# Kernel tuning notes

Measured on AMD Instinct MI355X. Metric: run time of the kernel, lower is better.

## Reference

```python
import jax, jax.numpy as jnp
import numpy as np


def setup_inputs() -> dict:
    key = jax.random.key(0)
    ks = jax.random.split(key, 10)
    N, E, IN, H, OUT = 100000, 1250000, 64, 128, 64
    inp = {
        "x": jax.random.normal(ks[0], (N, IN), dtype=jnp.float32),
        "edge_index": jax.random.randint(ks[1], (2, E), 0, N, dtype=jnp.int64),
        "W1x": jax.random.normal(ks[2], (IN, H), dtype=jnp.float32) * 0.1,
        "b1x": jnp.zeros((H,), jnp.float32),
        "W2x": jax.random.normal(ks[3], (H, H), dtype=jnp.float32) * 0.1,
        "b2x": jnp.zeros((H,), jnp.float32),
        "W1a": jax.random.normal(ks[4], (IN, H), dtype=jnp.float32) * 0.1,
        "b1a": jnp.zeros((H,), jnp.float32),
        "W2a": jax.random.normal(ks[5], (H, H), dtype=jnp.float32) * 0.1,
        "b2a": jnp.zeros((H,), jnp.float32),
        "Wc": jax.random.normal(ks[6], (2 * H, H), dtype=jnp.float32) * 0.1,
        "bc": jnp.zeros((H,), jnp.float32),
        "Wcls": jax.random.normal(ks[7], (H, OUT), dtype=jnp.float32) * 0.1,
        "bcls": jnp.zeros((OUT,), jnp.float32),
        "num_nodes": N,
    }
    return inp


def _normalize_adj(edge_index, num_nodes):
    # add self loops, then D^{-1/2} A D^{-1/2} edge weights (deg counted on rows)
    loops = jnp.arange(num_nodes, dtype=edge_index.dtype)
    ei = jnp.concatenate([edge_index, jnp.stack([loops, loops])], axis=1)
    row, col = ei[0], ei[1]
    deg = jax.ops.segment_sum(jnp.ones(row.shape[0], jnp.float32), row,
                              num_segments=num_nodes)
    dinv = jnp.where(deg > 0, jax.lax.rsqrt(deg), 0.0)
    ew = dinv[row] * dinv[col]
    return row, col, ew


def reference(x, edge_index, W1x, b1x, W2x, b2x, W1a, b1a, W2a, b2a,
              Wc, bc, Wcls, bcls, num_nodes):
    row, col, ew = _normalize_adj(edge_index, num_nodes)
    # sparse adjacency aggregation: gather, scale, scatter-add
    agg = jax.ops.segment_sum(x[col] * ew[:, None], row, num_segments=num_nodes)
    # dual-branch MLPs
    h_x = jax.nn.relu(x @ W1x + b1x) @ W2x + b2x
    h_a = jax.nn.relu(agg @ W1a + b1a) @ W2a + b2a
    h = jnp.concatenate([h_x, h_a], axis=1) @ Wc + bc
    h = jax.nn.relu(h)  # dropout: eval mode (identity)
    return h @ Wcls + bcls
```

## Files before the change

kernel.cpp:

```cpp
#include <hip/hip_runtime.h>
#include <stdint.h>

typedef unsigned short u16;
typedef unsigned int u32;
typedef __attribute__((ext_vector_type(8))) short frag_ab;
typedef __attribute__((ext_vector_type(4))) float f32x4;

__device__ __forceinline__ u16 f2b(float f) {
  unsigned u = __float_as_uint(f);
  return (u16)((u + 0x7fffu + ((u >> 16) & 1u)) >> 16);
}
__device__ __forceinline__ float b2f(u16 u) {
  return __uint_as_float(((unsigned)u) << 16);
}


__global__ void k_detect(const int* __restrict__ ei, int* __restrict__ flag) {
  int t = threadIdx.x;
  int v = ei[2 * t + 1];
  unsigned long long b = __ballot(v == 0);
  if (t == 0) *flag = (b == ~0ULL) ? 1 : 0;
}

__device__ __forceinline__ int edge_at(const void* ei, long pos, int is64) {
  if (is64) return (int)((const long long*)ei)[pos];
  return ((const int*)ei)[pos];
}

__global__ __launch_bounds__(256) void k_bhist_cvt(
    const void* __restrict__ ei, int E, int CH, int NB, int NBpad,
    int* __restrict__ bh, const int* __restrict__ flag,
    const float* __restrict__ x, u16* __restrict__ xb, long n64) {
  __shared__ int cnt[512];
  const int k = blockIdx.x, tid = threadIdx.x;
  for (long i = ((long)k * 256 + tid) * 8; i < n64; i += 65536L * 8) {
    float4 v0 = *(const float4*)(x + i);
    float4 v1 = *(const float4*)(x + i + 4);
    frag_ab o;
    o[0] = (short)f2b(v0.x); o[1] = (short)f2b(v0.y);
    o[2] = (short)f2b(v0.z); o[3] = (short)f2b(v0.w);
    o[4] = (short)f2b(v1.x); o[5] = (short)f2b(v1.y);
    o[6] = (short)f2b(v1.z); o[7] = (short)f2b(v1.w);
    *(frag_ab*)(xb + i) = o;
  }
  int is64 = *flag;
  for (int t = tid; t < NB; t += 256) cnt[t] = 0;
  __syncthreads();
  int e0 = k * CH, e1 = min(E, e0 + CH);
  for (int e = e0 + tid; e < e1; e += 256)
    atomicAdd(&cnt[edge_at(ei, e, is64) >> 9], 1);
  __syncthreads();
  for (int t = tid; t < NB; t += 256) bh[k * NBpad + t] = cnt[t];
}

__global__ __launch_bounds__(256) void k_cscan(
    int* __restrict__ bh, int* __restrict__ bstart, int NB, int NBpad, int E) {
  __shared__ int s[256];
  const int b = threadIdx.x;
  int tot = 0;
  if (b < NB)
    for (int k = 0; k < 256; ++k) tot += bh[k * NBpad + b];
  s[b] = (b < NB) ? tot : 0;
  __syncthreads();
  for (int off = 1; off < 256; off <<= 1) {
    int u = (b >= off) ? s[b - off] : 0;
    __syncthreads();
    s[b] += u;
    __syncthreads();
  }
  int excl = s[b] - tot;
  if (b < NB) {
    bstart[b] = excl;
    int run = excl;
    for (int k = 0; k < 256; ++k) {
      int t = bh[k * NBpad + b];
      bh[k * NBpad + b] = run;
      run += t;
    }
  }
  if (b == 0) bstart[NB] = E;
}

__global__ __launch_bounds__(256) void k_partition(
    const void* __restrict__ ei, int E, int CH, int NB, int NBpad,
    const int* __restrict__ bh, u32* __restrict__ staged,
    const int* __restrict__ flag) {
  __shared__ int cur[512];
  const int k = blockIdx.x, tid = threadIdx.x;
  int is64 = *flag;
  for (int t = tid; t < NB; t += 256) cur[t] = bh[k * NBpad + t];
  __syncthreads();
  int e0 = k * CH, e1 = min(E, e0 + CH);
  for (int e = e0 + tid; e < e1; e += 256) {
    int r = edge_at(ei, e, is64);
    int c = edge_at(ei, (long)E + e, is64);
    int pos = atomicAdd(&cur[r >> 9], 1);
    staged[pos] = ((u32)(r & 511) << 23) | (u32)c;
  }
}

__global__ __launch_bounds__(1024) void k_csr_bucket(
    const u32* __restrict__ staged, const int* __restrict__ bstart,
    int* __restrict__ rowptr, float* __restrict__ dinv,
    u32* __restrict__ cols, int N, int E) {
  __shared__ int cnt[512];
  __shared__ int cur[512];
  const int b = blockIdx.x, tid = threadIdx.x;
  const int r0 = b << 9;
  if (tid < 512) cnt[tid] = 0;
  __syncthreads();
  const int j0 = bstart[b], j1 = bstart[b + 1];
  for (int j = j0 + tid; j < j1; j += 1024)
    atomicAdd(&cnt[staged[j] >> 23], 1);
  __syncthreads();
  if (tid < 512) cur[tid] = cnt[tid];
  __syncthreads();
  for (int off = 1; off < 512; off <<= 1) {
    int v = 0;
    if (tid < 512 && tid >= off) v = cur[tid - off];
    __syncthreads();
    if (tid < 512) cur[tid] += v;
    __syncthreads();
  }
  int myStart = 0;
  if (tid < 512) {
    myStart = j0 + cur[tid] - cnt[tid];
    int r = r0 + tid;
    if (r < N) {
      rowptr[r] = myStart;
      dinv[r] = rsqrtf((float)cnt[tid] + 1.0f);
    }
  }
  __syncthreads();
  if (tid < 512) cur[tid] = myStart;
  if (b == 0 && tid == 0) rowptr[N] = E;
  __syncthreads();
  for (int j = j0 + tid; j < j1; j += 1024) {
    u32 v = staged[j];
    int rl = v >> 23;
    int pos = atomicAdd(&cur[rl], 1);
    cols[pos] = v & 0x7FFFFF;
  }
}

__global__ __launch_bounds__(256) void k_aggregate(
    const int* __restrict__ rowptr, const u32* __restrict__ cols,
    const u16* __restrict__ xb, const float* __restrict__ dinv,
    u16* __restrict__ aggb, int N) {
  int r = (blockIdx.x * 256 + threadIdx.x) >> 6;
  int f = threadIdx.x & 63;
  if (r >= N) return;
  int j = rowptr[r], end = rowptr[r + 1];
  float dr = dinv[r];
  float acc = b2f(xb[(long)r * 64 + f]) * dr;
  for (; j + 4 <= end; j += 4) {
    int c0 = cols[j], c1 = cols[j + 1], c2 = cols[j + 2], c3 = cols[j + 3];
    float w0 = dinv[c0], w1 = dinv[c1], w2 = dinv[c2], w3 = dinv[c3];
    float x0 = b2f(xb[(long)c0 * 64 + f]);
    float x1 = b2f(xb[(long)c1 * 64 + f]);
    float x2 = b2f(xb[(long)c2 * 64 + f]);
    float x3 = b2f(xb[(long)c3 * 64 + f]);
    acc = fmaf(x0, w0, acc);
    acc = fmaf(x1, w1, acc);
    acc = fmaf(x2, w2, acc);
    acc = fmaf(x3, w3, acc);
  }
  for (; j < end; ++j) {
    int c = cols[j];
    acc = fmaf(b2f(xb[(long)c * 64 + f]), dinv[c], acc);
  }
  aggb[(long)r * 64 + f] = f2b(acc * dr);
}

__global__ void k_wprod(const float* __restrict__ W2x, const float* __restrict__ W2a,
                        const float* __restrict__ Wc, const float* __restrict__ b2x,
                        const float* __restrict__ b2a, const float* __restrict__ bc,
                        float* __restrict__ Wxp, float* __restrict__ Wap,
                        float* __restrict__ bp) {
  int b = blockIdx.x, t = threadIdx.x;
  if (b < 128) {
    int j = t & 127;
    bool isX = (t < 128);
    const float* wrow = isX ? (W2x + b * 128) : (W2a + b * 128);
    const float* wc = isX ? Wc : (Wc + 128 * 128);
    float s = 0.f;
    for (int m = 0; m < 128; ++m) s = fmaf(wrow[m], wc[m * 128 + j], s);
    (isX ? Wxp : Wap)[b * 128 + j] = s;
  } else if (t < 128) {
    float s = bc[t];
    for (int m = 0; m < 128; ++m)
      s += b2x[m] * Wc[m * 128 + t] + b2a[m] * Wc[(128 + m) * 128 + t];
    bp[t] = s;
  }
}

__global__ void k_packall(
    const float* __restrict__ W1x, const float* __restrict__ W1a,
    const float* __restrict__ Wxp, const float* __restrict__ Wap,
    const float* __restrict__ Wcls,
    u16* __restrict__ W1xf, u16* __restrict__ W1af,
    u16* __restrict__ Wxpf, u16* __restrict__ Wapf, u16* __restrict__ Wclsf) {
  int blk = blockIdx.x;
  const float* W;
  u16* dst;
  int K, Nc, i0;
  if (blk < 32)       { W = W1x;  dst = W1xf;  K = 64;  Nc = 128; i0 = blk; }
  else if (blk < 64)  { W = W1a;  dst = W1af;  K = 64;  Nc = 128; i0 = blk - 32; }
  else if (blk < 128) { W = Wxp;  dst = Wxpf;  K = 128; Nc = 128; i0 = blk - 64; }
  else if (blk < 192) { W = Wap;  dst = Wapf;  K = 128; Nc = 128; i0 = blk - 128; }
  else                { W = Wcls; dst = Wclsf; K = 128; Nc = 64;  i0 = blk - 192; }
  int i = i0 * 256 + threadIdx.x;
  if (i >= K * Nc) return;
  int b = i & 7, l = (i >> 3) & 63, f = i >> 9;
  int KB = K >> 5;
  int kb = f % KB, nb = f / KB;
  int k = kb * 32 + (l >> 4) * 8 + b;
  int n = nb * 16 + (l & 15);
  dst[i] = f2b(W[k * Nc + n]);
}

__global__ __launch_bounds__(256) void k_mlp(
    const u16* __restrict__ xb, const u16* __restrict__ aggb,
    const u16* __restrict__ W1xf, const u16* __restrict__ W1af,
    const float* __restrict__ b1x, const float* __restrict__ b1a,
    const u16* __restrict__ Wxpf, const u16* __restrict__ Wapf,
    const float* __restrict__ bp,
    const u16* __restrict__ Wclsf, const float* __restrict__ bcls,
    float* __restrict__ out, int N) {
  __shared__ u16 H1[4][16 * 256];
  __shared__ u16 H2[4][16 * 128];
  const int w = threadIdx.x >> 6;
  const int lane = threadIdx.x & 63;
  const int m0 = blockIdx.x * 64 + w * 16;
  const int lm = lane & 15;
  const int lq = lane >> 4;
  u16* h1 = H1[w];
  u16* h2 = H2[w];

  for (int br = 0; br < 2; ++br) {
    const u16* A = br ? aggb : xb;
    const u16* Wf = br ? W1af : W1xf;
    const float* bias = br ? b1a : b1x;
    const u16* ap = A + (long)(m0 + lm) * 64 + lq * 8;
    frag_ab a0 = *(const frag_ab*)(ap);
    frag_ab a1 = *(const frag_ab*)(ap + 32);
#pragma unroll
    for (int nb = 0; nb < 8; ++nb) {
      frag_ab b0 = *(const frag_ab*)(Wf + (size_t)((nb * 2 + 0) * 64 + lane) * 8);
      frag_ab b1v = *(const frag_ab*)(Wf + (size_t)((nb * 2 + 1) * 64 + lane) * 8);
      f32x4 acc = {0.f, 0.f, 0.f, 0.f};
      acc = __builtin_amdgcn_mfma_f32_16x16x32_bf16(a0, b0, acc, 0, 0, 0);
      acc = __builtin_amdgcn_mfma_f32_16x16x32_bf16(a1, b1v, acc, 0, 0, 0);
      int col = nb * 16 + lm;
      float bv = bias[col];
#pragma unroll
      for (int r = 0; r < 4; ++r) {
        int row = lq * 4 + r;
        h1[(row * 256 + br * 128 + col) ^ ((row & 7) << 3)] =
            f2b(fmaxf(acc[r] + bv, 0.f));
      }
    }
  }
  __syncthreads();

  frag_ab hfr[8];
#pragma unroll
  for (int kb = 0; kb < 8; ++kb)
    hfr[kb] = *(const frag_ab*)&h1[(lm * 256 + kb * 32 + lq * 8) ^ ((lm & 7) << 3)];
#pragma unroll
  for (int nb = 0; nb < 8; ++nb) {
    f32x4 acc = {0.f, 0.f, 0.f, 0.f};
#pragma unroll
    for (int kb = 0; kb < 8; ++kb) {
      const u16* Wf2 = (kb < 4) ? Wxpf : Wapf;
      frag_ab b = *(const frag_ab*)(Wf2 + (size_t)((nb * 4 + (kb & 3)) * 64 + lane) * 8);
      acc = __builtin_amdgcn_mfma_f32_16x16x32_bf16(hfr[kb], b, acc, 0, 0, 0);
    }
    int col = nb * 16 + lm;
    float bv = bp[col];
#pragma unroll
    for (int r = 0; r < 4; ++r) {
      int row = lq * 4 + r;
      h2[(row * 128 + col) ^ ((row & 7) << 3)] = f2b(fmaxf(acc[r] + bv, 0.f));
    }
  }
  __syncthreads();

  frag_ab h3[4];
#pragma unroll
  for (int kb = 0; kb < 4; ++kb)
    h3[kb] = *(const frag_ab*)&h2[(lm * 128 + kb * 32 + lq * 8) ^ ((lm & 7) << 3)];
#pragma unroll
  for (int nb = 0; nb < 4; ++nb) {
    f32x4 acc = {0.f, 0.f, 0.f, 0.f};
#pragma unroll
    for (int kb = 0; kb < 4; ++kb) {
      frag_ab b = *(const frag_ab*)(Wclsf + (size_t)((nb * 4 + kb) * 64 + lane) * 8);
      acc = __builtin_amdgcn_mfma_f32_16x16x32_bf16(h3[kb], b, acc, 0, 0, 0);
    }
    int col = nb * 16 + lm;
    float bv = bcls[col];
#pragma unroll
    for (int r = 0; r < 4; ++r) {
      int grow = m0 + lq * 4 + r;
      if (grow < N) out[(long)grow * 64 + col] = acc[r] + bv;
    }
  }
}

extern "C" void kernel_launch(void* const* d_in, const int* in_sizes, int n_in,
                              void* d_out, int out_size, void* d_ws, size_t ws_size,
                              hipStream_t stream) {
  const float* x    = (const float*)d_in[0];
  const void*  ei   = d_in[1];
  const float* W1x  = (const float*)d_in[2];
  const float* b1x  = (const float*)d_in[3];
  const float* W2x  = (const float*)d_in[4];
  const float* b2x  = (const float*)d_in[5];
  const float* W1a  = (const float*)d_in[6];
  const float* b1a  = (const float*)d_in[7];
  const float* W2a  = (const float*)d_in[8];
  const float* b2a  = (const float*)d_in[9];
  const float* Wc   = (const float*)d_in[10];
  const float* bc   = (const float*)d_in[11];
  const float* Wcls = (const float*)d_in[12];
  const float* bcls = (const float*)d_in[13];
  const int N = in_sizes[0] / 64;
  const int E = in_sizes[1] / 2;

  const int NB = (N + 511) >> 9;
  const int NBpad = (NB + 63) & ~63;
  const int CH = (E + 255) / 256;

  float* ws = (float*)d_ws;
  long nAlign = (N + 255) & ~255L;
  float* dinv = ws;
  int*   rowptr = (int*)(ws + nAlign);
  int*   flag = (int*)(ws + 2 * nAlign + 256);
  u16*   xb   = (u16*)(ws + 2 * nAlign + 512);
  u16*   aggb = xb + (long)N * 64;
  float* Wxp  = (float*)(aggb + (long)N * 64);
  float* Wap  = Wxp + 16384;
  float* bp   = Wap + 16384;
  u16*   W1xf = (u16*)(bp + 128);
  u16*   W1af = W1xf + 8192;
  u16*   Wxpf = W1af + 8192;
  u16*   Wapf = Wxpf + 16384;
  u16*   Wclsf = Wapf + 16384;
  int*   bh   = (int*)(Wclsf + 8192);
  int*   bstart = bh + 256 * NBpad;
  u32*   staged = (u32*)(bstart + NB + 64);
  u32*   cols   = staged + E;
  float* out = (float*)d_out;

  k_detect<<<1, 64, 0, stream>>>((const int*)ei, flag);
  k_bhist_cvt<<<256, 256, 0, stream>>>(ei, E, CH, NB, NBpad, bh, flag,
                                       x, xb, (long)N * 64);
  k_cscan<<<1, 256, 0, stream>>>(bh, bstart, NB, NBpad, E);
  k_partition<<<256, 256, 0, stream>>>(ei, E, CH, NB, NBpad, bh, staged, flag);
  k_csr_bucket<<<NB, 1024, 0, stream>>>(staged, bstart, rowptr, dinv, cols, N, E);
  k_aggregate<<<(N * 64 + 255) / 256, 256, 0, stream>>>(rowptr, cols, xb, dinv, aggb, N);
  k_wprod<<<129, 256, 0, stream>>>(W2x, W2a, Wc, b2x, b2a, bc, Wxp, Wap, bp);
  k_packall<<<224, 256, 0, stream>>>(W1x, W1a, Wxp, Wap, Wcls,
                                     W1xf, W1af, Wxpf, Wapf, Wclsf);
  k_mlp<<<(N + 63) / 64, 256, 0, stream>>>(xb, aggb, W1xf, W1af, b1x, b1a,
                                           Wxpf, Wapf, bp, Wclsf, bcls, out, N);
}
```

Measured before the change: 172.8 us.

## Inline int64 detection, fuse weight product with packing, aggregate two rows per wave

Removes the separate detect kernel by having each edge-reading kernel probe the index width itself with a wave ballot. Merges the weight-product and packing kernels into one that writes packed bf16 directly, dropping the fp32 intermediates. The aggregation kernel now gives each wave two rows and interleaves their gathers to raise memory-level parallelism. Together this cuts two launches and should hide more gather latency, at the cost of extra registers and imbalance when the two rows differ in degree.

```diff
diff --git a/kernel.cpp b/kernel.cpp
--- a/kernel.cpp
+++ b/kernel.cpp
@@ -14,12 +14,10 @@
   return __uint_as_float(((unsigned)u) << 16);
 }
 
-
-__global__ void k_detect(const int* __restrict__ ei, int* __restrict__ flag) {
-  int t = threadIdx.x;
-  int v = ei[2 * t + 1];
+__device__ __forceinline__ int detect64(const int* __restrict__ ei32) {
+  int v = ei32[2 * (threadIdx.x & 63) + 1];
   unsigned long long b = __ballot(v == 0);
-  if (t == 0) *flag = (b == ~0ULL) ? 1 : 0;
+  return (b == ~0ULL) ? 1 : 0;
 }
 
 __device__ __forceinline__ int edge_at(const void* ei, long pos, int is64) {
@@ -29,10 +27,11 @@
 
 __global__ __launch_bounds__(256) void k_bhist_cvt(
     const void* __restrict__ ei, int E, int CH, int NB, int NBpad,
-    int* __restrict__ bh, const int* __restrict__ flag,
+    int* __restrict__ bh,
     const float* __restrict__ x, u16* __restrict__ xb, long n64) {
   __shared__ int cnt[512];
   const int k = blockIdx.x, tid = threadIdx.x;
+  const int is64 = detect64((const int*)ei);
   for (long i = ((long)k * 256 + tid) * 8; i < n64; i += 65536L * 8) {
     float4 v0 = *(const float4*)(x + i);
     float4 v1 = *(const float4*)(x + i + 4);
@@ -43,7 +42,6 @@
     o[6] = (short)f2b(v1.z); o[7] = (short)f2b(v1.w);
     *(frag_ab*)(xb + i) = o;
   }
-  int is64 = *flag;
   for (int t = tid; t < NB; t += 256) cnt[t] = 0;
   __syncthreads();
   int e0 = k * CH, e1 = min(E, e0 + CH);
@@ -83,11 +81,10 @@
 
 __global__ __launch_bounds__(256) void k_partition(
     const void* __restrict__ ei, int E, int CH, int NB, int NBpad,
-    const int* __restrict__ bh, u32* __restrict__ staged,
-    const int* __restrict__ flag) {
+    const int* __restrict__ bh, u32* __restrict__ staged) {
   __shared__ int cur[512];
   const int k = blockIdx.x, tid = threadIdx.x;
-  int is64 = *flag;
+  const int is64 = detect64((const int*)ei);
   for (int t = tid; t < NB; t += 256) cur[t] = bh[k * NBpad + t];
   __syncthreads();
   int e0 = k * CH, e1 = min(E, e0 + CH);
@@ -147,76 +144,113 @@
     const int* __restrict__ rowptr, const u32* __restrict__ cols,
     const u16* __restrict__ xb, const float* __restrict__ dinv,
     u16* __restrict__ aggb, int N) {
-  int r = (blockIdx.x * 256 + threadIdx.x) >> 6;
+  int q = (blockIdx.x * 256 + threadIdx.x) >> 6;
   int f = threadIdx.x & 63;
-  if (r >= N) return;
-  int j = rowptr[r], end = rowptr[r + 1];
-  float dr = dinv[r];
-  float acc = b2f(xb[(long)r * 64 + f]) * dr;
-  for (; j + 4 <= end; j += 4) {
-    int c0 = cols[j], c1 = cols[j + 1], c2 = cols[j + 2], c3 = cols[j + 3];
-    float w0 = dinv[c0], w1 = dinv[c1], w2 = dinv[c2], w3 = dinv[c3];
+  int r0 = q * 2, r1 = q * 2 + 1;
+  if (r0 >= N) return;
+  const bool has1 = (r1 < N);
+  int j0 = rowptr[r0], e0 = rowptr[r0 + 1];
+  int j1 = has1 ? rowptr[r1] : 0;
+  int e1 = has1 ? rowptr[r1 + 1] : 0;
+  float d0 = dinv[r0];
+  float d1 = has1 ? dinv[r1] : 0.f;
+  float acc0 = b2f(xb[(long)r0 * 64 + f]) * d0;
+  float acc1 = has1 ? b2f(xb[(long)r1 * 64 + f]) * d1 : 0.f;
+  while (j0 + 4 <= e0 && j1 + 4 <= e1) {
+    int ca0 = cols[j0], ca1 = cols[j0 + 1], ca2 = cols[j0 + 2], ca3 = cols[j0 + 3];
+    int cb0 = cols[j1], cb1 = cols[j1 + 1], cb2 = cols[j1 + 2], cb3 = cols[j1 + 3];
+    float xa0 = b2f(xb[(long)ca0 * 64 + f]);
+    float xa1 = b2f(xb[(long)ca1 * 64 + f]);
+    float xa2 = b2f(xb[(long)ca2 * 64 + f]);
+    float xa3 = b2f(xb[(long)ca3 * 64 + f]);
+    float xb0 = b2f(xb[(long)cb0 * 64 + f]);
+    float xb1 = b2f(xb[(long)cb1 * 64 + f]);
+    float xb2 = b2f(xb[(long)cb2 * 64 + f]);
+    float xb3 = b2f(xb[(long)cb3 * 64 + f]);
+    float wa0 = dinv[ca0], wa1 = dinv[ca1], wa2 = dinv[ca2], wa3 = dinv[ca3];
+    float wb0 = dinv[cb0], wb1 = dinv[cb1], wb2 = dinv[cb2], wb3 = dinv[cb3];
+    acc0 = fmaf(xa0, wa0, acc0); acc1 = fmaf(xb0, wb0, acc1);
+    acc0 = fmaf(xa1, wa1, acc0); acc1 = fmaf(xb1, wb1, acc1);
+    acc0 = fmaf(xa2, wa2, acc0); acc1 = fmaf(xb2, wb2, acc1);
+    acc0 = fmaf(xa3, wa3, acc0); acc1 = fmaf(xb3, wb3, acc1);
+    j0 += 4; j1 += 4;
+  }
+  for (; j0 + 4 <= e0; j0 += 4) {
+    int c0 = cols[j0], c1 = cols[j0 + 1], c2 = cols[j0 + 2], c3 = cols[j0 + 3];
     float x0 = b2f(xb[(long)c0 * 64 + f]);
     float x1 = b2f(xb[(long)c1 * 64 + f]);
     float x2 = b2f(xb[(long)c2 * 64 + f]);
     float x3 = b2f(xb[(long)c3 * 64 + f]);
-    acc = fmaf(x0, w0, acc);
-    acc = fmaf(x1, w1, acc);
-    acc = fmaf(x2, w2, acc);
-    acc = fmaf(x3, w3, acc);
-  }
-  for (; j < end; ++j) {
-    int c = cols[j];
-    acc = fmaf(b2f(xb[(long)c * 64 + f]), dinv[c], acc);
-  }
-  aggb[(long)r * 64 + f] = f2b(acc * dr);
-}
-
-__global__ void k_wprod(const float* __restrict__ W2x, const float* __restrict__ W2a,
-                        const float* __restrict__ Wc, const float* __restrict__ b2x,
-                        const float* __restrict__ b2a, const float* __restrict__ bc,
-                        float* __restrict__ Wxp, float* __restrict__ Wap,
-                        float* __restrict__ bp) {
-  int b = blockIdx.x, t = threadIdx.x;
-  if (b < 128) {
-    int j = t & 127;
-    bool isX = (t < 128);
-    const float* wrow = isX ? (W2x + b * 128) : (W2a + b * 128);
-    const float* wc = isX ? Wc : (Wc + 128 * 128);
+    acc0 = fmaf(x0, dinv[c0], acc0);
+    acc0 = fmaf(x1, dinv[c1], acc0);
+    acc0 = fmaf(x2, dinv[c2], acc0);
+    acc0 = fmaf(x3, dinv[c3], acc0);
+  }
+  for (; j0 < e0; ++j0) {
+    int c = cols[j0];
+    acc0 = fmaf(b2f(xb[(long)c * 64 + f]), dinv[c], acc0);
+  }
+  for (; j1 + 4 <= e1; j1 += 4) {
+    int c0 = cols[j1], c1 = cols[j1 + 1], c2 = cols[j1 + 2], c3 = cols[j1 + 3];
+    float x0 = b2f(xb[(long)c0 * 64 + f]);
+    float x1 = b2f(xb[(long)c1 * 64 + f]);
+    float x2 = b2f(xb[(long)c2 * 64 + f]);
+    float x3 = b2f(xb[(long)c3 * 64 + f]);
+    acc1 = fmaf(x0, dinv[c0], acc1);
+    acc1 = fmaf(x1, dinv[c1], acc1);
+    acc1 = fmaf(x2, dinv[c2], acc1);
+    acc1 = fmaf(x3, dinv[c3], acc1);
+  }
+  for (; j1 < e1; ++j1) {
+    int c = cols[j1];
+    acc1 = fmaf(b2f(xb[(long)c * 64 + f]), dinv[c], acc1);
+  }
+  aggb[(long)r0 * 64 + f] = f2b(acc0 * d0);
+  if (has1) aggb[(long)r1 * 64 + f] = f2b(acc1 * d1);
+}
+
+__global__ __launch_bounds__(256) void k_wpack(
+    const float* __restrict__ W1x, const float* __restrict__ W1a,
+    const float* __restrict__ W2x, const float* __restrict__ W2a,
+    const float* __restrict__ Wc, const float* __restrict__ b2x,
+    const float* __restrict__ b2a, const float* __restrict__ bc,
+    const float* __restrict__ Wcls,
+    u16* __restrict__ W1xf, u16* __restrict__ W1af,
+    u16* __restrict__ Wxpf, u16* __restrict__ Wapf,
+    u16* __restrict__ Wclsf, float* __restrict__ bp) {
+  const int blk = blockIdx.x, t = threadIdx.x;
+  if (blk < 128) {
+    const bool isX = blk < 64;
+    int i = (isX ? blk : blk - 64) * 256 + t;
+    const float* W2 = isX ? W2x : W2a;
+    const float* wc = isX ? Wc : Wc + 128 * 128;
+    int b = i & 7, l = (i >> 3) & 63, fi = i >> 9;
+    int kb = fi & 3, nb = fi >> 2;
+    int k = kb * 32 + (l >> 4) * 8 + b;
+    int n = nb * 16 + (l & 15);
     float s = 0.f;
-    for (int m = 0; m < 128; ++m) s = fmaf(wrow[m], wc[m * 128 + j], s);
-    (isX ? Wxp : Wap)[b * 128 + j] = s;
+    for (int m = 0; m < 128; ++m) s = fmaf(W2[k * 128 + m], wc[m * 128 + n], s);
+    (isX ? Wxpf : Wapf)[i] = f2b(s);
+  } else if (blk < 224) {
+    const float* W; u16* dst; int K, Nc, i0;
+    if (blk < 160)      { W = W1x;  dst = W1xf;  K = 64;  Nc = 128; i0 = blk - 128; }
+    else if (blk < 192) { W = W1a;  dst = W1af;  K = 64;  Nc = 128; i0 = blk - 160; }
+    else                { W = Wcls; dst = Wclsf; K = 128; Nc = 64;  i0 = blk - 192; }
+    int i = i0 * 256 + t;
+    if (i < K * Nc) {
+      int b = i & 7, l = (i >> 3) & 63, fi = i >> 9;
+      int KB = K >> 5;
+      int kb = fi % KB, nb = fi / KB;
+      int k = kb * 32 + (l >> 4) * 8 + b;
+      int n = nb * 16 + (l & 15);
+      dst[i] = f2b(W[k * Nc + n]);
+    }
   } else if (t < 128) {
     float s = bc[t];
     for (int m = 0; m < 128; ++m)
       s += b2x[m] * Wc[m * 128 + t] + b2a[m] * Wc[(128 + m) * 128 + t];
     bp[t] = s;
   }
-}
-
-__global__ void k_packall(
-    const float* __restrict__ W1x, const float* __restrict__ W1a,
-    const float* __restrict__ Wxp, const float* __restrict__ Wap,
-    const float* __restrict__ Wcls,
-    u16* __restrict__ W1xf, u16* __restrict__ W1af,
-    u16* __restrict__ Wxpf, u16* __restrict__ Wapf, u16* __restrict__ Wclsf) {
-  int blk = blockIdx.x;
-  const float* W;
-  u16* dst;
-  int K, Nc, i0;
-  if (blk < 32)       { W = W1x;  dst = W1xf;  K = 64;  Nc = 128; i0 = blk; }
-  else if (blk < 64)  { W = W1a;  dst = W1af;  K = 64;  Nc = 128; i0 = blk - 32; }
-  else if (blk < 128) { W = Wxp;  dst = Wxpf;  K = 128; Nc = 128; i0 = blk - 64; }
-  else if (blk < 192) { W = Wap;  dst = Wapf;  K = 128; Nc = 128; i0 = blk - 128; }
-  else                { W = Wcls; dst = Wclsf; K = 128; Nc = 64;  i0 = blk - 192; }
-  int i = i0 * 256 + threadIdx.x;
-  if (i >= K * Nc) return;
-  int b = i & 7, l = (i >> 3) & 63, f = i >> 9;
-  int KB = K >> 5;
-  int kb = f % KB, nb = f / KB;
-  int k = kb * 32 + (l >> 4) * 8 + b;
-  int n = nb * 16 + (l & 15);
-  dst[i] = f2b(W[k * Nc + n]);
 }
 
 __global__ __launch_bounds__(256) void k_mlp(
@@ -336,12 +370,9 @@
   long nAlign = (N + 255) & ~255L;
   float* dinv = ws;
   int*   rowptr = (int*)(ws + nAlign);
-  int*   flag = (int*)(ws + 2 * nAlign + 256);
-  u16*   xb   = (u16*)(ws + 2 * nAlign + 512);
+  u16*   xb   = (u16*)(ws + 2 * nAlign + 256);
   u16*   aggb = xb + (long)N * 64;
-  float* Wxp  = (float*)(aggb + (long)N * 64);
-  float* Wap  = Wxp + 16384;
-  float* bp   = Wap + 16384;
+  float* bp   = (float*)(aggb + (long)N * 64);
   u16*   W1xf = (u16*)(bp + 128);
   u16*   W1af = W1xf + 8192;
   u16*   Wxpf = W1af + 8192;
@@ -353,16 +384,13 @@
   u32*   cols   = staged + E;
   float* out = (float*)d_out;
 
-  k_detect<<<1, 64, 0, stream>>>((const int*)ei, flag);
-  k_bhist_cvt<<<256, 256, 0, stream>>>(ei, E, CH, NB, NBpad, bh, flag,
-                                       x, xb, (long)N * 64);
+  k_bhist_cvt<<<256, 256, 0, stream>>>(ei, E, CH, NB, NBpad, bh, x, xb, (long)N * 64);
   k_cscan<<<1, 256, 0, stream>>>(bh, bstart, NB, NBpad, E);
-  k_partition<<<256, 256, 0, stream>>>(ei, E, CH, NB, NBpad, bh, staged, flag);
+  k_partition<<<256, 256, 0, stream>>>(ei, E, CH, NB, NBpad, bh, staged);
   k_csr_bucket<<<NB, 1024, 0, stream>>>(staged, bstart, rowptr, dinv, cols, N, E);
-  k_aggregate<<<(N * 64 + 255) / 256, 256, 0, stream>>>(rowptr, cols, xb, dinv, aggb, N);
-  k_wprod<<<129, 256, 0, stream>>>(W2x, W2a, Wc, b2x, b2a, bc, Wxp, Wap, bp);
-  k_packall<<<224, 256, 0, stream>>>(W1x, W1a, Wxp, Wap, Wcls,
-                                     W1xf, W1af, Wxpf, Wapf, Wclsf);
+  k_aggregate<<<(N + 7) / 8, 256, 0, stream>>>(rowptr, cols, xb, dinv, aggb, N);
+  k_wpack<<<225, 256, 0, stream>>>(W1x, W1a, W2x, W2a, Wc, b2x, b2a, bc, Wcls,
+                                   W1xf, W1af, Wxpf, Wapf, Wclsf, bp);
   k_mlp<<<(N + 63) / 64, 256, 0, stream>>>(xb, aggb, W1xf, W1af, b1x, b1a,
                                            Wxpf, Wapf, bp, Wclsf, bcls, out, N);
 }
```

After: 157.7 us. 1.1x faster.
